# Kernel optimization log

Measured on AMD Instinct MI355X. Metric: run time of the kernel, lower is better.

Reference implementation:

```python
import jax, jax.numpy as jnp
import numpy as np


def setup_inputs() -> dict:
    key = jax.random.key(0)
    k1, k2 = jax.random.split(key)
    return {
        "embeddings": jax.random.normal(k1, (4, 768, 32, 32), dtype=jnp.float32),
        "database": jax.random.normal(k2, (20000, 768), dtype=jnp.float32),
        "k": 3,
        "out_h": 512,
        "out_w": 512,
    }


def reference(embeddings, database, k, out_h, out_w):
    # embeddings: [B, D, h, w]  (segmenter hidden state), database: [N, D]
    B, D, h, w = embeddings.shape
    # B x h x w x D -> B x (h*w) x D query layout, as in _get_ood_scores
    q = jnp.transpose(embeddings, (0, 2, 3, 1)).reshape(B, h * w, D)
    # squared Euclidean distances via (||q||^2 + ||x||^2 - 2 q.x)
    q2 = jnp.sum(q * q, axis=-1)[..., None]                 # [B, hw, 1]
    x2 = jnp.sum(database * database, axis=-1)[None, None]  # [1, 1, N]
    d2 = q2 + x2 - 2.0 * jnp.einsum("bqd,nd->bqn", q, database)
    dist = jnp.sqrt(jnp.maximum(d2, 1e-12))                 # [B, hw, N]
    # k smallest distances (sklearn kneighbors) then mean over neighbors
    neg_topk, _ = jax.lax.top_k(-dist, k)                   # [B, hw, k]
    ood = jnp.mean(-neg_topk, axis=-1).reshape(B, h, w)
    # F.interpolate(..., mode='bilinear', align_corners=False) == half-pixel bilinear
    ood_up = jax.image.resize(ood[:, None], (B, 1, out_h, out_w), method="bilinear")
    return ood_up
```

## Files before the change

kernel.cpp:

```cpp
#include <hip/hip_runtime.h>
#include <hip/hip_bf16.h>
#include <math.h>

constexpr int B    = 4;
constexpr int D    = 768;
constexpr int HW   = 1024;
constexpr int M    = B * HW;
constexpr int NDB  = 20000;
constexpr int LT   = 158;
constexpr int OUTH = 512;
constexpr int OUTW = 512;

constexpr int BM     = 256;
constexpr int BN     = 128;
constexpr int KSTEPS = D / 64;
constexpr int NSPLIT = 16;
constexpr int NT2    = 79;
constexpr int STEPB  = 128 * 64;

typedef int   i32x8  __attribute__((ext_vector_type(8)));
typedef float f32x16 __attribute__((ext_vector_type(16)));

__device__ __forceinline__ void insert3(float& t0, float& t1, float& t2, float d) {
    float a0 = fminf(d, t0);
    float b0 = fmaxf(d, t0);
    float a1 = fminf(b0, t1);
    float b1 = fmaxf(b0, t1);
    t0 = a0; t1 = a1;
    t2 = fminf(b1, t2);
}

__device__ __forceinline__ unsigned int pack4_fp8(float a, float b, float c, float d) {
    int v = __builtin_amdgcn_cvt_pk_fp8_f32(a, b, 0, false);
    v = __builtin_amdgcn_cvt_pk_fp8_f32(c, d, v, true);
    return (unsigned int)v;
}

__device__ __forceinline__ void gl_lds16(const unsigned char* g, unsigned char* l) {
    __builtin_amdgcn_global_load_lds(
        (const __attribute__((address_space(1))) void*)g,
        (__attribute__((address_space(3))) void*)l, 16, 0, 0);
}

__global__ __launch_bounds__(256) void convert_all(const float* __restrict__ db,
                                                   const float* __restrict__ emb,
                                                   uint4* __restrict__ dbt8,
                                                   uint4* __restrict__ qbt8,
                                                   float* __restrict__ x2p,
                                                   float* __restrict__ q2p) {
    __shared__ float panel[128][68];
    __shared__ float part[512];
    const int g = blockIdx.y;
    const int t = threadIdx.x;

    if (blockIdx.x < LT) {
        const int lt = blockIdx.x;
        const int n0 = lt * 128;

        #pragma unroll
        for (int pass = 0; pass < 8; ++pass) {
            int idx = pass * 256 + t;
            int row = idx >> 4, c4 = idx & 15;
            int n = n0 + row;
            float4 v = make_float4(0.f, 0.f, 0.f, 0.f);
            if (n < NDB) v = *(const float4*)(db + (size_t)n * D + g * 64 + c4 * 4);
            *(float4*)&panel[row][c4 * 4] = v;
        }
        __syncthreads();
        #pragma unroll
        for (int pass = 0; pass < 2; ++pass) {
            int idx = pass * 256 + t;
            int r  = idx & 31;
            int kc = (idx >> 5) & 1;
            int h2 = (idx >> 6) & 1;
            int rg = idx >> 7;
            int row  = rg * 32 + r;
            int kloc = kc * 32 + h2 * 16;
            float4 va = *(const float4*)&panel[row][kloc + 0];
            float4 vb = *(const float4*)&panel[row][kloc + 4];
            float4 vc = *(const float4*)&panel[row][kloc + 8];
            float4 vd = *(const float4*)&panel[row][kloc + 12];
            float ss = va.x*va.x + va.y*va.y + va.z*va.z + va.w*va.w
                     + vb.x*vb.x + vb.y*vb.y + vb.z*vb.z + vb.w*vb.w
                     + vc.x*vc.x + vc.y*vc.y + vc.z*vc.z + vc.w*vc.w
                     + vd.x*vd.x + vd.y*vd.y + vd.z*vd.z + vd.w*vd.w;
            uint4 o;
            o.x = pack4_fp8(va.x, va.y, va.z, va.w);
            o.y = pack4_fp8(vb.x, vb.y, vb.z, vb.w);
            o.z = pack4_fp8(vc.x, vc.y, vc.z, vc.w);
            o.w = pack4_fp8(vd.x, vd.y, vd.z, vd.w);
            dbt8[((size_t)lt * KSTEPS + g) * 512 + idx] = o;
            part[idx] = ss;
        }
        __syncthreads();
        if (t < 128) {
            int base = (t >> 5) * 128 + (t & 31);
            float s = part[base] + part[base + 32] + part[base + 64] + part[base + 96];
            x2p[((size_t)lt * KSTEPS + g) * 128 + t] = s;
        }
    } else {
        const int qt = blockIdx.x - LT;
        const int b  = qt >> 3;
        const int p0 = (qt & 7) * 128;

        #pragma unroll
        for (int pass = 0; pass < 2; ++pass) {
            int idx = pass * 256 + t;
            int r  = idx & 31;
            int kc = (idx >> 5) & 1;
            int h2 = (idx >> 6) & 1;
            int rg = idx >> 7;
            int prow = rg * 32 + r;
            int kb = g * 64 + kc * 32 + h2 * 16;
            const float* src = emb + ((size_t)b * D + kb) * HW + p0 + prow;
            float v[16];
            float ss = 0.f;
            #pragma unroll
            for (int j = 0; j < 16; ++j) {
                v[j] = src[(size_t)j * HW];
                ss = fmaf(v[j], v[j], ss);
            }
            uint4 o;
            o.x = pack4_fp8(-2.f*v[0],  -2.f*v[1],  -2.f*v[2],  -2.f*v[3]);
            o.y = pack4_fp8(-2.f*v[4],  -2.f*v[5],  -2.f*v[6],  -2.f*v[7]);
            o.z = pack4_fp8(-2.f*v[8],  -2.f*v[9],  -2.f*v[10], -2.f*v[11]);
            o.w = pack4_fp8(-2.f*v[12], -2.f*v[13], -2.f*v[14], -2.f*v[15]);
            qbt8[((size_t)qt * KSTEPS + g) * 512 + idx] = o;
            part[idx] = ss;
        }
        __syncthreads();
        if (t < 128) {
            int base = (t >> 5) * 128 + (t & 31);
            float s = part[base] + part[base + 32] + part[base + 64] + part[base + 96];
            q2p[((size_t)qt * KSTEPS + g) * 128 + t] = s;
        }
    }
}

__global__ __launch_bounds__(512, 4) void gemm_topk(const unsigned char* __restrict__ dbt8,
                                                    const unsigned char* __restrict__ qbt8,
                                                    const float* __restrict__ x2p,
                                                    float* __restrict__ partials) {
    __shared__ __align__(16) unsigned char Bsm[2 * 8192];
    __shared__ float red[4][BN][3];

    const int tid  = threadIdx.x;
    const int lane = tid & 63;
    const int w    = tid >> 6;
    const int r4   = w >> 1;
    const int c2   = w & 1;
    const int h    = lane >> 5;
    const int l31  = lane & 31;

    const int bid   = blockIdx.x;
    const int xcd   = bid & 7;
    const int j     = bid >> 3;
    const int sp    = xcd + 8 * (j >> 5);
    const int qtile = j & 31;
    const int m0    = qtile * BN;

    int b_off[2];
    #pragma unroll
    for (int jj = 0; jj < 2; ++jj) b_off[jj] = (2 * c2 + jj) * 2048 + h * 512 + l31 * 16;

    const unsigned char* aT = dbt8 + (size_t)(2 * sp + (r4 >> 1)) * KSTEPS * STEPB
                              + (r4 & 1) * 4096 + h * 512 + l31 * 16;

    const unsigned char* bQ = qbt8 + (size_t)qtile * KSTEPS * STEPB + w * 1024 + lane * 16;
    unsigned char* bD = Bsm + w * 1024;

    auto ldA = [&](i32x8& x0, i32x8& x1, const unsigned char* p) {
        int4 a = *(const int4*)(p);
        int4 b = *(const int4*)(p + 1024);
        int4 c = *(const int4*)(p + 2048);
        int4 d = *(const int4*)(p + 3072);
        x0 = (i32x8){a.x, a.y, a.z, a.w, b.x, b.y, b.z, b.w};
        x1 = (i32x8){c.x, c.y, c.z, c.w, d.x, d.y, d.z, d.w};
    };
    auto ldB = [&](i32x8& f, const unsigned char* Bb, int off) {
        int4 lo = *(const int4*)(Bb + off);
        int4 hi = *(const int4*)(Bb + off + 1024);
        f = (i32x8){lo.x, lo.y, lo.z, lo.w, hi.x, hi.y, hi.z, hi.w};
    };

    gl_lds16(bQ, bD);

    float t0[2], t1[2], t2[2];
    #pragma unroll
    for (int jj = 0; jj < 2; ++jj) { t0[jj] = INFINITY; t1[jj] = INFINITY; t2[jj] = INFINITY; }

    for (int tile = sp; tile < NT2; tile += NSPLIT) {
        const bool lastTile = (tile + NSPLIT >= NT2);

        float sx = 1e30f;
        {
            int n = tile * BM + r4 * 64 + lane;
            if (n < NDB) {
                const float* p = x2p + (size_t)(n >> 7) * (KSTEPS * 128) + (n & 127);
                sx = 0.f;
                #pragma unroll
                for (int g = 0; g < KSTEPS; ++g) sx += p[g * 128];
            }
        }

        f32x16 acc[2][2];
        #pragma unroll
        for (int i = 0; i < 2; ++i)
            #pragma unroll
            for (int jj = 0; jj < 2; ++jj)
                #pragma unroll
                for (int r = 0; r < 16; ++r) acc[i][jj][r] = 0.f;

        #pragma unroll 2
        for (int g = 0; g < KSTEPS; ++g) {
            __syncthreads();

            i32x8 af0, af1;
            ldA(af0, af1, aT + g * STEPB);

            if (g + 1 < KSTEPS) {
                gl_lds16(bQ + (g + 1) * STEPB, bD + ((g + 1) & 1) * 8192);
            } else if (!lastTile) {
                gl_lds16(bQ, bD);
            }

            const unsigned char* Bb = Bsm + (g & 1) * 8192;
            i32x8 bf0, bf1;
            ldB(bf0, Bb, b_off[0]);
            ldB(bf1, Bb, b_off[1]);

            acc[0][0] = __builtin_amdgcn_mfma_scale_f32_32x32x64_f8f6f4(
                af0, bf0, acc[0][0], 0, 0, 0, 0x7f7f7f7f, 0, 0x7f7f7f7f);
            acc[1][0] = __builtin_amdgcn_mfma_scale_f32_32x32x64_f8f6f4(
                af1, bf0, acc[1][0], 0, 0, 0, 0x7f7f7f7f, 0, 0x7f7f7f7f);
            acc[0][1] = __builtin_amdgcn_mfma_scale_f32_32x32x64_f8f6f4(
                af0, bf1, acc[0][1], 0, 0, 0, 0x7f7f7f7f, 0, 0x7f7f7f7f);
            acc[1][1] = __builtin_amdgcn_mfma_scale_f32_32x32x64_f8f6f4(
                af1, bf1, acc[1][1], 0, 0, 0, 0x7f7f7f7f, 0, 0x7f7f7f7f);
        }
        aT += (size_t)2 * NSPLIT * KSTEPS * STEPB;

        #pragma unroll
        for (int i = 0; i < 2; ++i) {
            #pragma unroll
            for (int rg2 = 0; rg2 < 4; ++rg2) {
                #pragma unroll
                for (int rr = 0; rr < 4; ++rr) {
                    float xv = __shfl(sx, i * 32 + rg2 * 8 + 4 * h + rr);
                    #pragma unroll
                    for (int jj = 0; jj < 2; ++jj)
                        insert3(t0[jj], t1[jj], t2[jj], acc[i][jj][rg2 * 4 + rr] + xv);
                }
            }
        }
    }

    #pragma unroll
    for (int jj = 0; jj < 2; ++jj) {
        float o0 = __shfl_xor(t0[jj], 32);
        float o1 = __shfl_xor(t1[jj], 32);
        float o2 = __shfl_xor(t2[jj], 32);
        insert3(t0[jj], t1[jj], t2[jj], o0);
        insert3(t0[jj], t1[jj], t2[jj], o1);
        insert3(t0[jj], t1[jj], t2[jj], o2);
    }
    if (h == 0) {
        #pragma unroll
        for (int jj = 0; jj < 2; ++jj) {
            int col = (2 * c2 + jj) * 32 + l31;
            red[r4][col][0] = t0[jj];
            red[r4][col][1] = t1[jj];
            red[r4][col][2] = t2[jj];
        }
    }
    __syncthreads();
    if (tid < BN) {
        float a0 = red[0][tid][0], a1 = red[0][tid][1], a2 = red[0][tid][2];
        #pragma unroll
        for (int ww = 1; ww < 4; ++ww) {
            insert3(a0, a1, a2, red[ww][tid][0]);
            insert3(a0, a1, a2, red[ww][tid][1]);
            insert3(a0, a1, a2, red[ww][tid][2]);
        }
        float* dst = partials + ((size_t)(m0 + tid) * NSPLIT + sp) * 3;
        dst[0] = a0; dst[1] = a1; dst[2] = a2;
    }
}

__global__ __launch_bounds__(256) void merge_ood(const float* __restrict__ partials,
                                                 const float* __restrict__ q2p,
                                                 float* __restrict__ ood) {
    int m = blockIdx.x * 256 + threadIdx.x;
    if (m >= M) return;
    const float* pp = partials + (size_t)m * NSPLIT * 3;
    float a0 = INFINITY, a1 = INFINITY, a2 = INFINITY;
    #pragma unroll
    for (int j = 0; j < NSPLIT * 3; ++j) insert3(a0, a1, a2, pp[j]);
    const float* qp = q2p + (size_t)(m >> 7) * KSTEPS * 128 + (m & 127);
    float q = 0.f;
    #pragma unroll
    for (int g = 0; g < KSTEPS; ++g) q += qp[g * 128];
    float d0 = sqrtf(fmaxf(q + a0, 1e-12f));
    float d1 = sqrtf(fmaxf(q + a1, 1e-12f));
    float d2 = sqrtf(fmaxf(q + a2, 1e-12f));
    ood[m] = (d0 + d1 + d2) * (1.f / 3.f);
}

__global__ __launch_bounds__(256) void upsample(const float* __restrict__ ood,
                                                float* __restrict__ out) {
    int idx = blockIdx.x * 256 + threadIdx.x;
    int ox = idx & (OUTW - 1);
    int oy = (idx >> 9) & (OUTH - 1);
    int bb = idx >> 18;
    float sx = (ox + 0.5f) * (32.f / OUTW) - 0.5f;
    float sy = (oy + 0.5f) * (32.f / OUTH) - 0.5f;
    float fx = floorf(sx), fy = floorf(sy);
    float wx = sx - fx, wy = sy - fy;
    int x0 = max(0, min(31, (int)fx));
    int x1 = max(0, min(31, (int)fx + 1));
    int y0 = max(0, min(31, (int)fy));
    int y1 = max(0, min(31, (int)fy + 1));
    const float* src = ood + bb * 1024;
    float v00 = src[y0 * 32 + x0];
    float v01 = src[y0 * 32 + x1];
    float v10 = src[y1 * 32 + x0];
    float v11 = src[y1 * 32 + x1];
    float top = v00 + wx * (v01 - v00);
    float bot = v10 + wx * (v11 - v10);
    out[idx] = top + wy * (bot - top);
}

extern "C" void kernel_launch(void* const* d_in, const int* in_sizes, int n_in,
                              void* d_out, int out_size, void* d_ws, size_t ws_size,
                              hipStream_t stream) {
    const float* emb = (const float*)d_in[0];
    const float* db  = (const float*)d_in[1];
    float* out = (float*)d_out;

    char* ws = (char*)d_ws;
    unsigned char* dbt8 = (unsigned char*)ws;
    unsigned char* qbt8 = (unsigned char*)(ws + 15532032);
    float* x2p      = (float*)(ws + 18677760);
    float* q2p      = (float*)(ws + 19648512);
    float* ood      = (float*)(ws + 19845120);
    float* partials = (float*)(ws + 19861504);

    convert_all<<<dim3(LT + 32, KSTEPS), 256, 0, stream>>>(db, emb, (uint4*)dbt8,
                                                           (uint4*)qbt8, x2p, q2p);
    gemm_topk<<<NSPLIT * 32, 512, 0, stream>>>(dbt8, qbt8, x2p, partials);
    merge_ood<<<(M + 255) / 256, 256, 0, stream>>>(partials, q2p, ood);
    upsample<<<(B * OUTH * OUTW) / 256, 256, 0, stream>>>(ood, out);
}
```

Measured before the change: 193.4 us.

## Shrink GEMM-topk tiles to 128x64 with 4-stage LDS ring and A prefetch

Halves the block tile (BM 256→128, BN 128→64), uses 256-thread blocks and launches twice as many blocks, so each wave computes one 32-row A slice against two B fragments. Query tiles now go through a 4-slot LDS ring loaded two steps ahead with a barrier every other k-step, and the next A fragment is register-prefetched. The x2 norm load moves after the MFMA loop. The aim is more blocks for better CU occupancy and load balance, and fewer barriers and less load latency per step. In exchange, each block reuses less data and there are more partial writes.

Measured after the change: 195.1 us. Within noise of the previous version (+0.9%).

```diff
diff --git a/kernel.cpp b/kernel.cpp
--- a/kernel.cpp
+++ b/kernel.cpp
@@ -11,11 +11,11 @@
 constexpr int OUTH = 512;
 constexpr int OUTW = 512;
 
-constexpr int BM     = 256;
-constexpr int BN     = 128;
+constexpr int BM     = 128;
+constexpr int BN     = 64;
 constexpr int KSTEPS = D / 64;
 constexpr int NSPLIT = 16;
-constexpr int NT2    = 79;
+constexpr int NT     = 158;
 constexpr int STEPB  = 128 * 64;
 
 typedef int   i32x8  __attribute__((ext_vector_type(8)));
@@ -137,120 +137,106 @@
     }
 }
 
-__global__ __launch_bounds__(512, 4) void gemm_topk(const unsigned char* __restrict__ dbt8,
+__global__ __launch_bounds__(256, 4) void gemm_topk(const unsigned char* __restrict__ dbt8,
                                                     const unsigned char* __restrict__ qbt8,
                                                     const float* __restrict__ x2p,
                                                     float* __restrict__ partials) {
-    __shared__ __align__(16) unsigned char Bsm[2 * 8192];
+    __shared__ __align__(16) unsigned char Bsm[4 * 4096];
     __shared__ float red[4][BN][3];
 
     const int tid  = threadIdx.x;
     const int lane = tid & 63;
     const int w    = tid >> 6;
-    const int r4   = w >> 1;
-    const int c2   = w & 1;
     const int h    = lane >> 5;
     const int l31  = lane & 31;
 
-    const int bid   = blockIdx.x;
-    const int xcd   = bid & 7;
-    const int j     = bid >> 3;
-    const int sp    = xcd + 8 * (j >> 5);
-    const int qtile = j & 31;
-    const int m0    = qtile * BN;
-
-    int b_off[2];
-    #pragma unroll
-    for (int jj = 0; jj < 2; ++jj) b_off[jj] = (2 * c2 + jj) * 2048 + h * 512 + l31 * 16;
-
-    const unsigned char* aT = dbt8 + (size_t)(2 * sp + (r4 >> 1)) * KSTEPS * STEPB
-                              + (r4 & 1) * 4096 + h * 512 + l31 * 16;
-
-    const unsigned char* bQ = qbt8 + (size_t)qtile * KSTEPS * STEPB + w * 1024 + lane * 16;
-    unsigned char* bD = Bsm + w * 1024;
-
-    auto ldA = [&](i32x8& x0, i32x8& x1, const unsigned char* p) {
-        int4 a = *(const int4*)(p);
-        int4 b = *(const int4*)(p + 1024);
-        int4 c = *(const int4*)(p + 2048);
-        int4 d = *(const int4*)(p + 3072);
-        x0 = (i32x8){a.x, a.y, a.z, a.w, b.x, b.y, b.z, b.w};
-        x1 = (i32x8){c.x, c.y, c.z, c.w, d.x, d.y, d.z, d.w};
-    };
-    auto ldB = [&](i32x8& f, const unsigned char* Bb, int off) {
-        int4 lo = *(const int4*)(Bb + off);
-        int4 hi = *(const int4*)(Bb + off + 1024);
+    const int bid = blockIdx.x;
+    const int xcd = bid & 7;
+    const int j   = bid >> 3;
+    const int sp  = xcd + 8 * (j >> 6);
+    const int q64 = j & 63;
+    const int m0  = q64 * BN;
+
+    const int b_off0 = 0 * 2048 + h * 512 + l31 * 16;
+    const int b_off1 = 1 * 2048 + h * 512 + l31 * 16;
+
+    const unsigned char* aW = dbt8 + (size_t)sp * KSTEPS * STEPB
+                              + w * 2048 + h * 512 + l31 * 16;
+
+    const unsigned char* bQ = qbt8 + (size_t)(q64 >> 1) * KSTEPS * STEPB
+                              + (q64 & 1) * 4096 + w * 1024 + lane * 16;
+
+    auto ldF = [&](i32x8& f, const unsigned char* p) {
+        int4 lo = *(const int4*)(p);
+        int4 hi = *(const int4*)(p + 1024);
         f = (i32x8){lo.x, lo.y, lo.z, lo.w, hi.x, hi.y, hi.z, hi.w};
     };
 
-    gl_lds16(bQ, bD);
+    gl_lds16(bQ,         Bsm + 0 * 4096 + w * 1024);
+    gl_lds16(bQ + STEPB, Bsm + 1 * 4096 + w * 1024);
 
     float t0[2], t1[2], t2[2];
     #pragma unroll
     for (int jj = 0; jj < 2; ++jj) { t0[jj] = INFINITY; t1[jj] = INFINITY; t2[jj] = INFINITY; }
 
-    for (int tile = sp; tile < NT2; tile += NSPLIT) {
-        const bool lastTile = (tile + NSPLIT >= NT2);
+    for (int tile = sp; tile < NT; tile += NSPLIT) {
+        const bool lastTile = (tile + NSPLIT >= NT);
+
+        f32x16 acc0, acc1;
+        #pragma unroll
+        for (int r = 0; r < 16; ++r) { acc0[r] = 0.f; acc1[r] = 0.f; }
+
+        i32x8 af, an;
+        ldF(af, aW);
+
+        #pragma unroll 2
+        for (int g = 0; g < KSTEPS; ++g) {
+            if ((g & 1) == 0) __syncthreads();
+
+            {
+                int gs = g + 2;
+                unsigned char* dst = Bsm + ((g + 2) & 3) * 4096 + w * 1024;
+                if (gs < KSTEPS) {
+                    gl_lds16(bQ + (size_t)gs * STEPB, dst);
+                } else if (!lastTile) {
+                    gl_lds16(bQ + (size_t)(gs - KSTEPS) * STEPB, dst);
+                }
+            }
+
+            if (g + 1 < KSTEPS) ldF(an, aW + (size_t)(g + 1) * STEPB);
+
+            const unsigned char* Bb = Bsm + (g & 3) * 4096;
+            i32x8 bf0, bf1;
+            ldF(bf0, Bb + b_off0);
+            ldF(bf1, Bb + b_off1);
+
+            acc0 = __builtin_amdgcn_mfma_scale_f32_32x32x64_f8f6f4(
+                af, bf0, acc0, 0, 0, 0, 0x7f7f7f7f, 0, 0x7f7f7f7f);
+            acc1 = __builtin_amdgcn_mfma_scale_f32_32x32x64_f8f6f4(
+                af, bf1, acc1, 0, 0, 0, 0x7f7f7f7f, 0, 0x7f7f7f7f);
+
+            af = an;
+        }
+        aW += (size_t)NSPLIT * KSTEPS * STEPB;
 
         float sx = 1e30f;
         {
-            int n = tile * BM + r4 * 64 + lane;
+            int n = tile * BM + w * 32 + l31;
             if (n < NDB) {
-                const float* p = x2p + (size_t)(n >> 7) * (KSTEPS * 128) + (n & 127);
+                const float* p = x2p + (size_t)tile * (KSTEPS * 128) + w * 32 + l31;
                 sx = 0.f;
                 #pragma unroll
                 for (int g = 0; g < KSTEPS; ++g) sx += p[g * 128];
             }
         }
 
-        f32x16 acc[2][2];
-        #pragma unroll
-        for (int i = 0; i < 2; ++i)
+        #pragma unroll
+        for (int rg2 = 0; rg2 < 4; ++rg2) {
             #pragma unroll
-            for (int jj = 0; jj < 2; ++jj)
-                #pragma unroll
-                for (int r = 0; r < 16; ++r) acc[i][jj][r] = 0.f;
-
-        #pragma unroll 2
-        for (int g = 0; g < KSTEPS; ++g) {
-            __syncthreads();
-
-            i32x8 af0, af1;
-            ldA(af0, af1, aT + g * STEPB);
-
-            if (g + 1 < KSTEPS) {
-                gl_lds16(bQ + (g + 1) * STEPB, bD + ((g + 1) & 1) * 8192);
-            } else if (!lastTile) {
-                gl_lds16(bQ, bD);
-            }
-
-            const unsigned char* Bb = Bsm + (g & 1) * 8192;
-            i32x8 bf0, bf1;
-            ldB(bf0, Bb, b_off[0]);
-            ldB(bf1, Bb, b_off[1]);
-
-            acc[0][0] = __builtin_amdgcn_mfma_scale_f32_32x32x64_f8f6f4(
-                af0, bf0, acc[0][0], 0, 0, 0, 0x7f7f7f7f, 0, 0x7f7f7f7f);
-            acc[1][0] = __builtin_amdgcn_mfma_scale_f32_32x32x64_f8f6f4(
-                af1, bf0, acc[1][0], 0, 0, 0, 0x7f7f7f7f, 0, 0x7f7f7f7f);
-            acc[0][1] = __builtin_amdgcn_mfma_scale_f32_32x32x64_f8f6f4(
-                af0, bf1, acc[0][1], 0, 0, 0, 0x7f7f7f7f, 0, 0x7f7f7f7f);
-            acc[1][1] = __builtin_amdgcn_mfma_scale_f32_32x32x64_f8f6f4(
-                af1, bf1, acc[1][1], 0, 0, 0, 0x7f7f7f7f, 0, 0x7f7f7f7f);
-        }
-        aT += (size_t)2 * NSPLIT * KSTEPS * STEPB;
-
-        #pragma unroll
-        for (int i = 0; i < 2; ++i) {
-            #pragma unroll
-            for (int rg2 = 0; rg2 < 4; ++rg2) {
-                #pragma unroll
-                for (int rr = 0; rr < 4; ++rr) {
-                    float xv = __shfl(sx, i * 32 + rg2 * 8 + 4 * h + rr);
-                    #pragma unroll
-                    for (int jj = 0; jj < 2; ++jj)
-                        insert3(t0[jj], t1[jj], t2[jj], acc[i][jj][rg2 * 4 + rr] + xv);
-                }
+            for (int rr = 0; rr < 4; ++rr) {
+                float xv = __shfl(sx, rg2 * 8 + 4 * h + rr);
+                insert3(t0[0], t1[0], t2[0], acc0[rg2 * 4 + rr] + xv);
+                insert3(t0[1], t1[1], t2[1], acc1[rg2 * 4 + rr] + xv);
             }
         }
     }
@@ -267,10 +253,10 @@
     if (h == 0) {
         #pragma unroll
         for (int jj = 0; jj < 2; ++jj) {
-            int col = (2 * c2 + jj) * 32 + l31;
-            red[r4][col][0] = t0[jj];
-            red[r4][col][1] = t1[jj];
-            red[r4][col][2] = t2[jj];
+            int col = jj * 32 + l31;
+            red[w][col][0] = t0[jj];
+            red[w][col][1] = t1[jj];
+            red[w][col][2] = t2[jj];
         }
     }
     __syncthreads();
@@ -347,7 +333,7 @@
 
     convert_all<<<dim3(LT + 32, KSTEPS), 256, 0, stream>>>(db, emb, (uint4*)dbt8,
                                                            (uint4*)qbt8, x2p, q2p);
-    gemm_topk<<<NSPLIT * 32, 512, 0, stream>>>(dbt8, qbt8, x2p, partials);
+    gemm_topk<<<NSPLIT * 64, 256, 0, stream>>>(dbt8, qbt8, x2p, partials);
     merge_ood<<<(M + 255) / 256, 256, 0, stream>>>(partials, q2p, ood);
     upsample<<<(B * OUTH * OUTW) / 256, 256, 0, stream>>>(ood, out);
 }
```
